# Kernel optimization log

Measured on AMD Instinct MI355X. Metric: run time of the kernel, lower is better.

Reference implementation:

```python
import jax, jax.numpy as jnp
import numpy as np

B, S, H, E, K, DFF = 4, 2048, 1024, 8, 2, 4096


def setup_inputs() -> dict:
    key = jax.random.key(0)
    k0, k1, k2, k3 = jax.random.split(key, 4)
    sc = 0.02
    return {
        "x": jax.random.normal(k0, (B, S, H), jnp.float32),
        "gate_W": jax.random.normal(k1, (H, E), jnp.float32) * sc,
        "gate_b": jnp.zeros((E,), jnp.float32),
        "W1": jax.random.normal(k2, (H, DFF), jnp.float32) * sc,
        "b1": jnp.zeros((DFF,), jnp.float32),
        "W2": jax.random.normal(k3, (DFF, H), jnp.float32) * sc,
        "b2": jnp.zeros((H,), jnp.float32),
    }


def reference(x, gate_W, gate_b, W1, b1, W2, b2):
    b, s, h = x.shape
    x_flat = x.reshape(-1, h)                      # [T, H]
    gate_scores = x_flat @ gate_W + gate_b         # [T, E]
    top_k_scores, top_k_idx = jax.lax.top_k(gate_scores, K)   # [T, K]
    top_k_w = jax.nn.softmax(top_k_scores, axis=-1)           # [T, K]

    # All experts share the same weights (ModuleList reuses one module), so
    # sum_i w_i * expert_i(x) == expert(x) * sum_i w_i. top_k indices are
    # unique per token, so the per-token combine weight is sum of top-k weights.
    hdd = jax.nn.gelu(x_flat @ W1 + b1, approximate=False)    # [T, DFF]
    y = hdd @ W2 + b2                                         # [T, H]
    tok_w = top_k_w.sum(axis=-1)                              # [T] (== 1.0)
    output = (y * tok_w[:, None]).reshape(b, s, h)

    expert_load = gate_scores.mean(axis=0)                    # [E]
    aux_loss = (expert_load ** 2).sum()
    exp_counts = jnp.zeros((E,), jnp.int32).at[top_k_idx.ravel()].add(1)
    return output, aux_loss, exp_counts
```

## Files before the change

### kernel.cpp

```cpp
#include <hip/hip_runtime.h>
#include <hip/hip_bf16.h>
#include <math.h>

#define Tn   8192
#define Hn   1024
#define En   8
#define DFFn 4096

typedef __attribute__((ext_vector_type(8))) short bf16x8;
typedef __attribute__((ext_vector_type(4))) float f32x4;

static __device__ inline unsigned short f2bf(float f) {
    __hip_bfloat16 h = __float2bfloat16(f);
    return __builtin_bit_cast(unsigned short, h);
}

__global__ __launch_bounds__(256) void prep(
    const float* __restrict__ W1, unsigned short* __restrict__ W1t,
    const float* __restrict__ W2, unsigned short* __restrict__ W2t,
    const float* __restrict__ x, const float* __restrict__ gW,
    const float* __restrict__ gb, unsigned short* __restrict__ xbf,
    float* __restrict__ tokw, float* __restrict__ load_sum,
    int* __restrict__ counts)
{
    __shared__ float smem[8 * 1024 + En];
    __shared__ int   s_cnt[En];
    const int tid = threadIdx.x;
    const int id  = blockIdx.x;

    if (id >= 5120) {
        const int tb = id - 5120;
        float* tile = smem;
        const int bx = tb & 31, by = tb >> 5;
        const int n0 = bx * 32, k0 = by * 32;
        const int r  = tid >> 3, c4 = (tid & 7) * 4;
        float4 v = *(const float4*)(W2 + (size_t)(k0 + r) * Hn + n0 + c4);
        tile[(c4 + 0) * 33 + r] = v.x;
        tile[(c4 + 1) * 33 + r] = v.y;
        tile[(c4 + 2) * 33 + r] = v.z;
        tile[(c4 + 3) * 33 + r] = v.w;
        __syncthreads();
        ushort4 pk;
        pk.x = f2bf(tile[r * 33 + c4 + 0]);
        pk.y = f2bf(tile[r * 33 + c4 + 1]);
        pk.z = f2bf(tile[r * 33 + c4 + 2]);
        pk.w = f2bf(tile[r * 33 + c4 + 3]);
        *(ushort4*)(W2t + (size_t)(n0 + r) * DFFn + k0 + c4) = pk;
        return;
    }

    if (id >= 1024) {
        const int tb = id - 1024;
        float* tile = smem;
        const int bx = tb & 127, by = tb >> 7;
        const int n0 = bx * 32, k0 = by * 32;
        const int r  = tid >> 3, c4 = (tid & 7) * 4;
        float4 v = *(const float4*)(W1 + (size_t)(k0 + r) * DFFn + n0 + c4);
        tile[(c4 + 0) * 33 + r] = v.x;
        tile[(c4 + 1) * 33 + r] = v.y;
        tile[(c4 + 2) * 33 + r] = v.z;
        tile[(c4 + 3) * 33 + r] = v.w;
        __syncthreads();
        ushort4 pk;
        pk.x = f2bf(tile[r * 33 + c4 + 0]);
        pk.y = f2bf(tile[r * 33 + c4 + 1]);
        pk.z = f2bf(tile[r * 33 + c4 + 2]);
        pk.w = f2bf(tile[r * 33 + c4 + 3]);
        *(ushort4*)(W1t + (size_t)(n0 + r) * Hn + k0 + c4) = pk;
        return;
    }

    float* gwt    = smem;
    float* s_load = smem + 8 * 1024;
    if (tid < En) { s_load[tid] = 0.f; s_cnt[tid] = 0; }
    #pragma unroll
    for (int i = 0; i < 32; ++i) {
        int f = tid + i * 256;
        gwt[(f & 7) * 1024 + (f >> 3)] = gW[f];
    }
    __syncthreads();

    const int lane = tid & 63;
    const int wv   = tid >> 6;

    for (int tok = id * 4 + wv; tok < Tn; tok += 4096) {
        const float4* xr = (const float4*)(x + (size_t)tok * Hn);
        float acc[8] = {0.f,0.f,0.f,0.f,0.f,0.f,0.f,0.f};
        #pragma unroll
        for (int j = 0; j < Hn / 256; ++j) {
            int h4 = j * 64 + lane;
            float4 xv = xr[h4];
            ushort4 pk;
            pk.x = f2bf(xv.x); pk.y = f2bf(xv.y);
            pk.z = f2bf(xv.z); pk.w = f2bf(xv.w);
            ((ushort4*)xbf)[(size_t)tok * (Hn / 4) + h4] = pk;
            #pragma unroll
            for (int e = 0; e < 8; ++e) {
                const float4 w = *(const float4*)(gwt + e * 1024 + h4 * 4);
                acc[e] += xv.x * w.x + xv.y * w.y + xv.z * w.z + xv.w * w.w;
            }
        }
        #pragma unroll
        for (int e = 0; e < 8; ++e) {
            float v = acc[e];
            #pragma unroll
            for (int off = 32; off > 0; off >>= 1) v += __shfl_xor(v, off, 64);
            acc[e] = v + gb[e];
        }
        if (lane == 0) {
            #pragma unroll
            for (int e = 0; e < 8; ++e) atomicAdd(&s_load[e], acc[e]);
            int i1 = 0; float v1 = acc[0];
            #pragma unroll
            for (int e = 1; e < 8; ++e) if (acc[e] > v1) { v1 = acc[e]; i1 = e; }
            int i2 = -1; float v2 = -3.0e38f;
            #pragma unroll
            for (int e = 0; e < 8; ++e) if (e != i1 && acc[e] > v2) { v2 = acc[e]; i2 = e; }
            atomicAdd(&s_cnt[i1], 1);
            atomicAdd(&s_cnt[i2], 1);
            float e2 = __expf(v2 - v1);
            float t  = 1.0f + e2;
            tokw[tok] = 1.0f / t + e2 / t;
        }
    }
    __syncthreads();
    if (tid < En) {
        atomicAdd(&load_sum[tid], s_load[tid]);
        atomicAdd(&counts[tid],   s_cnt[tid]);
    }
}


static __device__ inline bf16x8 ldsfrag(const char* base, int row, int chunk) {
    return *(const bf16x8*)(base + row * 128 + (((chunk) ^ (row & 7)) << 4));
}

template<int BN, int WM, int WN, int EPI>
__global__ __launch_bounds__(512, 2) void gemm8(
    const __hip_bfloat16* __restrict__ A,
    const __hip_bfloat16* __restrict__ Bt,
    const float* __restrict__ bias,
    const float* __restrict__ tokw,
    void* __restrict__ C, int N, int K, int nx,
    const float* __restrict__ load_sum, const int* __restrict__ counts,
    float* __restrict__ out_tail, int nblk)
{
    constexpr int BM = 256;
    constexpr int MR = (BM / WM) / 16;
    constexpr int NR = (BN / WN) / 16;
    constexpr int AU = BM / 64;
    constexpr int BU = BN / 64;
    constexpr int ABYTES = BM * 64 * 2;
    constexpr int BBYTES = BN * 64 * 2;
    constexpr int TILEB  = ABYTES + BBYTES;

    extern __shared__ char lds[];

    const int tid = threadIdx.x;
    const int id  = blockIdx.x;

    if (EPI == 0 && id >= nblk) {
        if (tid == 0) {
            float aux = 0.f;
            #pragma unroll
            for (int e = 0; e < En; ++e) {
                float m = load_sum[e] * (1.0f / (float)Tn);
                aux += m * m;
            }
            out_tail[0] = aux;
            #pragma unroll
            for (int e = 0; e < En; ++e) out_tail[1 + e] = (float)counts[e];
        }
        return;
    }

    int wg = id;
    { int xcd = wg & 7, idx = wg >> 3; wg = xcd * (nblk >> 3) + idx; }
    const int by = wg / nx, bx = wg % nx;
    const int m0 = by * BM, n0 = bx * BN;

    const int lane = tid & 63;
    const int wid  = tid >> 6;
    const int wn   = wid % WN;
    const int wm   = wid / WN;
    const int wrow = wm * (BM / WM);
    const int wcol = wn * (BN / WN);
    const int fr   = lane & 15;
    const int fq   = lane >> 4;

    const int sr = tid >> 3;
    const int sc = (tid & 7) ^ (sr & 7);
    unsigned aOff[AU], bOff[BU];
    #pragma unroll
    for (int u = 0; u < AU; ++u)
        aOff[u] = (unsigned)((m0 + u * 64 + sr) * K + sc * 8);
    #pragma unroll
    for (int u = 0; u < BU; ++u)
        bOff[u] = (unsigned)((n0 + u * 64 + sr) * K + sc * 8);

#define STA(b, u, kt) __builtin_amdgcn_global_load_lds( \
    (const __attribute__((address_space(1))) void*)(A + aOff[u] + (unsigned)(kt) * 64u), \
    (__attribute__((address_space(3))) void*)(lds + (b) * TILEB + (u) * 8192 + tid * 16), 16, 0, 0)
#define STB(b, u, kt) __builtin_amdgcn_global_load_lds( \
    (const __attribute__((address_space(1))) void*)(Bt + bOff[u] + (unsigned)(kt) * 64u), \
    (__attribute__((address_space(3))) void*)(lds + (b) * TILEB + ABYTES + (u) * 8192 + tid * 16), 16, 0, 0)

    bf16x8 af[MR / 2][2];
    bf16x8 bfr[4][2];
    f32x4  acc[MR][NR];
    const f32x4 zero = {0.f, 0.f, 0.f, 0.f};
    #pragma unroll
    for (int i = 0; i < MR; ++i)
        #pragma unroll
        for (int j = 0; j < NR; ++j) acc[i][j] = zero;

#define RDA(b, half) do { _Pragma("unroll") \
    for (int m_ = 0; m_ < MR / 2; ++m_) { _Pragma("unroll") \
        for (int ks_ = 0; ks_ < 2; ++ks_) \
            af[m_][ks_] = ldsfrag(lds + (b) * TILEB, \
                wrow + ((half) * (MR / 2) + m_) * 16 + fr, ks_ * 4 + fq); } } while (0)

#define RDB(b, half) do { _Pragma("unroll") \
    for (int n_ = 0; n_ < 2; ++n_) { _Pragma("unroll") \
        for (int ks_ = 0; ks_ < 2; ++ks_) \
            bfr[(half) * 2 + n_][ks_] = ldsfrag(lds + (b) * TILEB + ABYTES, \
                wcol + ((half) * 2 + n_) * 16 + fr, ks_ * 4 + fq); } } while (0)

#define MFMAQ(hm, hn) do { \
    __builtin_amdgcn_s_setprio(1); \
    _Pragma("unroll") \
    for (int m_ = 0; m_ < MR / 2; ++m_) { _Pragma("unroll") \
        for (int n_ = 0; n_ < 2; ++n_) { _Pragma("unroll") \
            for (int ks_ = 0; ks_ < 2; ++ks_) \
                acc[(hm) * (MR / 2) + m_][(hn) * 2 + n_] = \
                    __builtin_amdgcn_mfma_f32_16x16x32_bf16( \
                        af[m_][ks_], bfr[(hn) * 2 + n_][ks_], \
                        acc[(hm) * (MR / 2) + m_][(hn) * 2 + n_], 0, 0, 0); } } \
    __builtin_amdgcn_s_setprio(0); } while (0)

#define MIDSYNC do { \
    __builtin_amdgcn_sched_barrier(0); \
    __builtin_amdgcn_s_barrier(); \
    asm volatile("s_waitcnt lgkmcnt(0)" ::: "memory"); \
    __builtin_amdgcn_sched_barrier(0); } while (0)

#define ENDBAR do { \
    __builtin_amdgcn_sched_barrier(0); \
    __builtin_amdgcn_s_barrier(); \
    __builtin_amdgcn_sched_barrier(0); } while (0)

#define DRAIN do { \
    if constexpr (WM == 2) asm volatile("s_waitcnt vmcnt(6)" ::: "memory"); \
    else                   asm volatile("s_waitcnt vmcnt(4)" ::: "memory"); \
    __builtin_amdgcn_sched_barrier(0); } while (0)

    const int KT = K >> 6;

    if constexpr (WM == 2) {
        STA(0,0,0); STA(0,1,0); STA(0,2,0); STA(0,3,0);
        STB(0,0,0); STB(0,1,0); STB(0,2,0); STB(0,3,0);
        STA(1,0,1); STA(1,2,1);
        STB(1,0,1); STB(1,1,1); STB(1,2,1); STB(1,3,1);
        asm volatile("s_waitcnt vmcnt(6)" ::: "memory");
    } else {
        STA(0,0,0); STA(0,1,0); STA(0,2,0); STA(0,3,0);
        STB(0,0,0); STB(0,1,0);
        STA(1,0,1); STA(1,1,1);
        STB(1,0,1); STB(1,1,1);
        asm volatile("s_waitcnt vmcnt(4)" ::: "memory");
    }
    __builtin_amdgcn_sched_barrier(0);
    __builtin_amdgcn_s_barrier();
    __builtin_amdgcn_sched_barrier(0);

    for (int i = 0; i < (KT >> 1); ++i) {
        const int t1 = 2 * i + 1;
        const int c2 = (2 * i + 2 < KT) ? 2 * i + 2 : KT - 1;
        const int c3 = (2 * i + 3 < KT) ? 2 * i + 3 : KT - 1;

        RDA(0, 0); RDB(0, 0);
        if constexpr (WM == 2) { STA(1,1,t1); STA(1,3,t1); }
        else                   { STA(1,2,t1); STA(1,3,t1); }
        MIDSYNC; MFMAQ(0, 0); ENDBAR;
        RDB(0, 1);
        if constexpr (WM == 2) { STA(0,0,c2); STA(0,2,c2); }
        MIDSYNC; MFMAQ(0, 1); ENDBAR;
        RDA(0, 1);
        STB(0,0,c2); STB(0,1,c2);
        MIDSYNC; MFMAQ(1, 0); ENDBAR;
        if constexpr (WM == 2) { STB(0,2,c2); STB(0,3,c2); }
        else                   { STA(0,0,c2); STA(0,1,c2); }
        MIDSYNC; MFMAQ(1, 1); DRAIN; ENDBAR;
        RDA(1, 0); RDB(1, 0);
        if constexpr (WM == 2) { STA(0,1,c2); STA(0,3,c2); }
        else                   { STA(0,2,c2); STA(0,3,c2); }
        MIDSYNC; MFMAQ(0, 0); ENDBAR;
        RDB(1, 1);
        if constexpr (WM == 2) { STA(1,0,c3); STA(1,2,c3); }
        MIDSYNC; MFMAQ(0, 1); ENDBAR;
        RDA(1, 1);
        STB(1,0,c3); STB(1,1,c3);
        MIDSYNC; MFMAQ(1, 0); ENDBAR;
        if constexpr (WM == 2) { STB(1,2,c3); STB(1,3,c3); }
        else                   { STA(1,0,c3); STA(1,1,c3); }
        MIDSYNC; MFMAQ(1, 1); DRAIN; ENDBAR;
    }

    #pragma unroll
    for (int mi = 0; mi < MR; ++mi) {
        #pragma unroll
        for (int ni = 0; ni < NR; ++ni) {
            const int col   = n0 + wcol + ni * 16 + (lane & 15);
            const int rbase = m0 + wrow + mi * 16 + (lane >> 4) * 4;
            const float bv  = bias[col];
            #pragma unroll
            for (int i2 = 0; i2 < 4; ++i2) {
                const int row = rbase + i2;
                float v = acc[mi][ni][i2] + bv;
                if constexpr (EPI == 0) {
                    float vv = v * v;
                    float z  = v * __fmaf_rn(vv, -0.07135607f, -1.59576912f);
                    float e  = __expf(z);
                    float g  = v * __builtin_amdgcn_rcpf(1.0f + e);
                    ((__hip_bfloat16*)C)[(size_t)row * N + col] = __float2bfloat16(g);
                } else {
                    ((float*)C)[(size_t)row * N + col] = v * tokw[row];
                }
            }
        }
    }

#undef STA
#undef STB
#undef RDA
#undef RDB
#undef MFMAQ
#undef MIDSYNC
#undef ENDBAR
#undef DRAIN
}

extern "C" void kernel_launch(void* const* d_in, const int* in_sizes, int n_in,
                              void* d_out, int out_size, void* d_ws, size_t ws_size,
                              hipStream_t stream)
{
    const float* x  = (const float*)d_in[0];
    const float* gW = (const float*)d_in[1];
    const float* gb = (const float*)d_in[2];
    const float* W1 = (const float*)d_in[3];
    const float* b1 = (const float*)d_in[4];
    const float* W2 = (const float*)d_in[5];
    const float* b2 = (const float*)d_in[6];
    float* out = (float*)d_out;

    char* ws = (char*)d_ws;
    __hip_bfloat16* xbf = (__hip_bfloat16*)ws;  ws += (size_t)Tn * Hn * 2;
    __hip_bfloat16* W1t = (__hip_bfloat16*)ws;  ws += (size_t)Hn * DFFn * 2;
    __hip_bfloat16* W2t = (__hip_bfloat16*)ws;  ws += (size_t)Hn * DFFn * 2;
    __hip_bfloat16* hdd = (__hip_bfloat16*)ws;  ws += (size_t)Tn * DFFn * 2;
    float* tokw     = (float*)ws;               ws += (size_t)Tn * 4;
    float* load_sum = (float*)ws;               ws += En * 4;
    int*   counts   = (int*)ws;                 ws += En * 4;

    static bool attr_done = false;
    if (!attr_done) {
        (void)hipFuncSetAttribute(
            reinterpret_cast<const void*>(&gemm8<256, 2, 4, 0>),
            hipFuncAttributeMaxDynamicSharedMemorySize, 131072);
        (void)hipFuncSetAttribute(
            reinterpret_cast<const void*>(&gemm8<128, 4, 2, 1>),
            hipFuncAttributeMaxDynamicSharedMemorySize, 98304);
        attr_done = true;
    }

    hipMemsetAsync(load_sum, 0, En * 4 * 2, stream);

    prep<<<9216, 256, 0, stream>>>(W1, (unsigned short*)W1t,
                                   W2, (unsigned short*)W2t,
                                   x, gW, gb, (unsigned short*)xbf,
                                   tokw, load_sum, counts);

    gemm8<256, 2, 4, 0><<<513, 512, 131072, stream>>>(
        xbf, W1t, b1, nullptr, hdd, DFFn, Hn, 16,
        load_sum, counts, out + (size_t)Tn * Hn, 512);

    gemm8<128, 4, 2, 1><<<256, 512, 98304, stream>>>(
        hdd, W2t, b2, tokw, out, Hn, DFFn, 8,
        nullptr, nullptr, nullptr, 256);
}
```

Measured before the change: 270.1 us.

## Swap MFMA operands for row-major vector epilogue and restructure WM=1 pipeline

```diff
diff --git a/kernel.cpp b/kernel.cpp
--- a/kernel.cpp
+++ b/kernel.cpp
@@ -234,8 +234,20 @@
             for (int ks_ = 0; ks_ < 2; ++ks_) \
                 acc[(hm) * (MR / 2) + m_][(hn) * 2 + n_] = \
                     __builtin_amdgcn_mfma_f32_16x16x32_bf16( \
-                        af[m_][ks_], bfr[(hn) * 2 + n_][ks_], \
+                        bfr[(hn) * 2 + n_][ks_], af[m_][ks_], \
                         acc[(hm) * (MR / 2) + m_][(hn) * 2 + n_], 0, 0, 0); } } \
+    __builtin_amdgcn_s_setprio(0); } while (0)
+
+#define MFMAQ1(hm) do { \
+    __builtin_amdgcn_s_setprio(1); \
+    _Pragma("unroll") \
+    for (int m_ = 0; m_ < MR / 2; ++m_) { _Pragma("unroll") \
+        for (int n_ = 0; n_ < NR; ++n_) { _Pragma("unroll") \
+            for (int ks_ = 0; ks_ < 2; ++ks_) \
+                acc[(hm) * (MR / 2) + m_][n_] = \
+                    __builtin_amdgcn_mfma_f32_16x16x32_bf16( \
+                        bfr[n_][ks_], af[m_][ks_], \
+                        acc[(hm) * (MR / 2) + m_][n_], 0, 0, 0); } } \
     __builtin_amdgcn_s_setprio(0); } while (0)
 
 #define MIDSYNC do { \
@@ -249,9 +261,9 @@
     __builtin_amdgcn_s_barrier(); \
     __builtin_amdgcn_sched_barrier(0); } while (0)
 
-#define DRAIN do { \
-    if constexpr (WM == 2) asm volatile("s_waitcnt vmcnt(6)" ::: "memory"); \
-    else                   asm volatile("s_waitcnt vmcnt(4)" ::: "memory"); \
+#define DRAIN6 do { asm volatile("s_waitcnt vmcnt(6)" ::: "memory"); \
+    __builtin_amdgcn_sched_barrier(0); } while (0)
+#define DRAIN2 do { asm volatile("s_waitcnt vmcnt(2)" ::: "memory"); \
     __builtin_amdgcn_sched_barrier(0); } while (0)
 
     const int KT = K >> 6;
@@ -261,71 +273,101 @@
         STB(0,0,0); STB(0,1,0); STB(0,2,0); STB(0,3,0);
         STA(1,0,1); STA(1,2,1);
         STB(1,0,1); STB(1,1,1); STB(1,2,1); STB(1,3,1);
-        asm volatile("s_waitcnt vmcnt(6)" ::: "memory");
+        DRAIN6;
+        __builtin_amdgcn_s_barrier();
+        __builtin_amdgcn_sched_barrier(0);
+
+        for (int i = 0; i < (KT >> 1); ++i) {
+            const int t1 = 2 * i + 1;
+            const int c2 = (2 * i + 2 < KT) ? 2 * i + 2 : KT - 1;
+            const int c3 = (2 * i + 3 < KT) ? 2 * i + 3 : KT - 1;
+
+            RDA(0, 0); RDB(0, 0);
+            STA(1,1,t1); STA(1,3,t1);
+            MIDSYNC; MFMAQ(0, 0); ENDBAR;
+            RDB(0, 1);
+            STA(0,0,c2); STA(0,2,c2);
+            MIDSYNC; MFMAQ(0, 1); ENDBAR;
+            RDA(0, 1);
+            STB(0,0,c2); STB(0,1,c2);
+            MIDSYNC; MFMAQ(1, 0); ENDBAR;
+            STB(0,2,c2); STB(0,3,c2);
+            MIDSYNC; MFMAQ(1, 1); DRAIN6; ENDBAR;
+            RDA(1, 0); RDB(1, 0);
+            STA(0,1,c2); STA(0,3,c2);
+            MIDSYNC; MFMAQ(0, 0); ENDBAR;
+            RDB(1, 1);
+            STA(1,0,c3); STA(1,2,c3);
+            MIDSYNC; MFMAQ(0, 1); ENDBAR;
+            RDA(1, 1);
+            STB(1,0,c3); STB(1,1,c3);
+            MIDSYNC; MFMAQ(1, 0); ENDBAR;
+            STB(1,2,c3); STB(1,3,c3);
+            MIDSYNC; MFMAQ(1, 1); DRAIN6; ENDBAR;
+        }
     } else {
         STA(0,0,0); STA(0,1,0); STA(0,2,0); STA(0,3,0);
         STB(0,0,0); STB(0,1,0);
-        STA(1,0,1); STA(1,1,1);
         STB(1,0,1); STB(1,1,1);
-        asm volatile("s_waitcnt vmcnt(4)" ::: "memory");
-    }
-    __builtin_amdgcn_sched_barrier(0);
-    __builtin_amdgcn_s_barrier();
-    __builtin_amdgcn_sched_barrier(0);
-
-    for (int i = 0; i < (KT >> 1); ++i) {
-        const int t1 = 2 * i + 1;
-        const int c2 = (2 * i + 2 < KT) ? 2 * i + 2 : KT - 1;
-        const int c3 = (2 * i + 3 < KT) ? 2 * i + 3 : KT - 1;
-
-        RDA(0, 0); RDB(0, 0);
-        if constexpr (WM == 2) { STA(1,1,t1); STA(1,3,t1); }
-        else                   { STA(1,2,t1); STA(1,3,t1); }
-        MIDSYNC; MFMAQ(0, 0); ENDBAR;
-        RDB(0, 1);
-        if constexpr (WM == 2) { STA(0,0,c2); STA(0,2,c2); }
-        MIDSYNC; MFMAQ(0, 1); ENDBAR;
-        RDA(0, 1);
-        STB(0,0,c2); STB(0,1,c2);
-        MIDSYNC; MFMAQ(1, 0); ENDBAR;
-        if constexpr (WM == 2) { STB(0,2,c2); STB(0,3,c2); }
-        else                   { STA(0,0,c2); STA(0,1,c2); }
-        MIDSYNC; MFMAQ(1, 1); DRAIN; ENDBAR;
-        RDA(1, 0); RDB(1, 0);
-        if constexpr (WM == 2) { STA(0,1,c2); STA(0,3,c2); }
-        else                   { STA(0,2,c2); STA(0,3,c2); }
-        MIDSYNC; MFMAQ(0, 0); ENDBAR;
-        RDB(1, 1);
-        if constexpr (WM == 2) { STA(1,0,c3); STA(1,2,c3); }
-        MIDSYNC; MFMAQ(0, 1); ENDBAR;
-        RDA(1, 1);
-        STB(1,0,c3); STB(1,1,c3);
-        MIDSYNC; MFMAQ(1, 0); ENDBAR;
-        if constexpr (WM == 2) { STB(1,2,c3); STB(1,3,c3); }
-        else                   { STA(1,0,c3); STA(1,1,c3); }
-        MIDSYNC; MFMAQ(1, 1); DRAIN; ENDBAR;
-    }
+        DRAIN2;
+        __builtin_amdgcn_s_barrier();
+        __builtin_amdgcn_sched_barrier(0);
+
+        for (int i = 0; i < (KT >> 1); ++i) {
+            const int t1 = 2 * i + 1;
+            const int c2 = (2 * i + 2 < KT) ? 2 * i + 2 : KT - 1;
+            const int c3 = (2 * i + 3 < KT) ? 2 * i + 3 : KT - 1;
+
+            RDA(0, 0); RDB(0, 0); RDB(0, 1);
+            STA(1,0,t1); STA(1,1,t1); STA(1,2,t1); STA(1,3,t1);
+            MIDSYNC; MFMAQ1(0); ENDBAR;
+            RDA(0, 1);
+            STB(0,0,c2); STB(0,1,c2);
+            MIDSYNC; MFMAQ1(1); DRAIN2; ENDBAR;
+            RDA(1, 0); RDB(1, 0); RDB(1, 1);
+            STA(0,0,c2); STA(0,1,c2); STA(0,2,c2); STA(0,3,c2);
+            MIDSYNC; MFMAQ1(0); ENDBAR;
+            RDA(1, 1);
+            STB(1,0,c3); STB(1,1,c3);
+            MIDSYNC; MFMAQ1(1); DRAIN2; ENDBAR;
+        }
+    }
+
+    const int mrow0 = m0 + wrow + (lane & 15);
+    const int ncol0 = n0 + wcol + (lane >> 4) * 4;
+    float4 b4[NR];
+    #pragma unroll
+    for (int ni = 0; ni < NR; ++ni)
+        b4[ni] = *(const float4*)(bias + ncol0 + ni * 16);
 
     #pragma unroll
     for (int mi = 0; mi < MR; ++mi) {
+        const int row = mrow0 + mi * 16;
+        float tw = 1.0f;
+        if constexpr (EPI == 1) tw = tokw[row];
         #pragma unroll
         for (int ni = 0; ni < NR; ++ni) {
-            const int col   = n0 + wcol + ni * 16 + (lane & 15);
-            const int rbase = m0 + wrow + mi * 16 + (lane >> 4) * 4;
-            const float bv  = bias[col];
-            #pragma unroll
-            for (int i2 = 0; i2 < 4; ++i2) {
-                const int row = rbase + i2;
-                float v = acc[mi][ni][i2] + bv;
-                if constexpr (EPI == 0) {
-                    float vv = v * v;
-                    float z  = v * __fmaf_rn(vv, -0.07135607f, -1.59576912f);
+            const int cb = ncol0 + ni * 16;
+            f32x4 v = acc[mi][ni];
+            v[0] += b4[ni].x; v[1] += b4[ni].y;
+            v[2] += b4[ni].z; v[3] += b4[ni].w;
+            if constexpr (EPI == 0) {
+                ushort4 pk;
+                #pragma unroll
+                for (int j = 0; j < 4; ++j) {
+                    float u  = v[j];
+                    float uu = u * u;
+                    float z  = u * __fmaf_rn(uu, -0.07135607f, -1.59576912f);
                     float e  = __expf(z);
-                    float g  = v * __builtin_amdgcn_rcpf(1.0f + e);
-                    ((__hip_bfloat16*)C)[(size_t)row * N + col] = __float2bfloat16(g);
-                } else {
-                    ((float*)C)[(size_t)row * N + col] = v * tokw[row];
+                    float g  = u * __builtin_amdgcn_rcpf(1.0f + e);
+                    ((unsigned short*)&pk)[j] = f2bf(g);
                 }
+                *(ushort4*)((__hip_bfloat16*)C + (size_t)row * N + cb) = pk;
+            } else {
+                float4 o;
+                o.x = v[0] * tw; o.y = v[1] * tw;
+                o.z = v[2] * tw; o.w = v[3] * tw;
+                *(float4*)((float*)C + (size_t)row * N + cb) = o;
             }
         }
     }
@@ -335,9 +377,11 @@
 #undef RDA
 #undef RDB
 #undef MFMAQ
+#undef MFMAQ1
 #undef MIDSYNC
 #undef ENDBAR
-#undef DRAIN
+#undef DRAIN6
+#undef DRAIN2
 }
 
 extern "C" void kernel_launch(void* const* d_in, const int* in_sizes, int n_in,
```

Result: slower. 277.2 us (+2.6%).
